# Kernel optimization log

Measured on AMD Instinct MI355X. Metric: run time of the kernel, lower is better.

Reference implementation:

```python
import jax, jax.numpy as jnp
import numpy as np

BATCH, T, N = 64, 512, 1024

def setup_inputs() -> dict:
    key = jax.random.key(0)
    k1, k2, k3 = jax.random.split(key, 3)
    input_sequence = jax.random.normal(k1, (BATCH, T, N), dtype=jnp.float32)
    W_self_lower = jax.random.normal(k2, (N, N), dtype=jnp.float32) * 0.1
    W_input = jax.random.normal(k3, (N, N), dtype=jnp.float32) * 0.1
    return {"input_sequence": input_sequence, "W_self_lower": W_self_lower, "W_input": W_input}

def reference(input_sequence, W_self_lower, W_input):
    # W_self symmetric: (W + W.T)/2; note W_self.T == W_self
    W_self = (W_self_lower + W_self_lower.T) * 0.5
    batch = input_sequence.shape[0]
    n = W_self.shape[0]
    # Precompute input projection for all timesteps: (B, T, N) @ (N, N)^T
    x_proj = jnp.einsum('btn,mn->btm', input_sequence, W_input)
    h0 = jnp.zeros((batch, n), dtype=input_sequence.dtype)

    def step(h, xp_t):
        h_new = jnp.tanh(h @ W_self.T + xp_t)
        return h_new, h_new

    # scan over time axis: move T to leading axis
    _, states = jax.lax.scan(step, h0, jnp.swapaxes(x_proj, 0, 1))
    return jnp.swapaxes(states, 0, 1)  # (B, T, N)
```

## Files before the change

kernel.cpp:

```cpp
#include <hip/hip_runtime.h>
#include <cstdint>
#include <cmath>

constexpr int BATCH = 64;
constexpr int T     = 512;
constexpr int N     = 1024;
constexpr int NWG   = 256;
constexpr int NG    = 32;
constexpr int GM    = 16;

typedef float f4 __attribute__((ext_vector_type(4)));
typedef float f2 __attribute__((ext_vector_type(2)));

struct alignas(128) PadInt { int v; int pad[31]; };
__device__ PadInt g_cnt[NG];
__device__ PadInt g_flag[NG];

__device__ __forceinline__ f4 ld_sys_x4(const float* p) {
  f4 v;
  asm volatile("global_load_dwordx4 %0, %1, off sc0 sc1" : "=v"(v) : "v"(p));
  return v;
}
__device__ __forceinline__ int ld_sys_i32(const int* p) {
  int v;
  asm volatile("global_load_dword %0, %1, off sc0 sc1\n\ts_waitcnt vmcnt(0)"
               : "=v"(v) : "v"(p) : "memory");
  return v;
}
__device__ __forceinline__ void st_sys_x2(float* p, f2 v) {
  asm volatile("global_store_dwordx2 %0, %1, off sc0 sc1 nt" ::"v"(p), "v"(v)
               : "memory");
}
__device__ __forceinline__ void wait_vm0(void) {
  asm volatile("s_waitcnt vmcnt(0)" ::: "memory");
  __builtin_amdgcn_sched_barrier(0);
}

__device__ __forceinline__ void arrive_cnt(int g, int t) {
  int old = __hip_atomic_fetch_add(&g_cnt[g].v, 1, __ATOMIC_RELAXED,
                                   __HIP_MEMORY_SCOPE_AGENT);
  if (old == t * GM + (GM - 1))
    __hip_atomic_store(&g_flag[g].v, t + 1, __ATOMIC_RELAXED,
                       __HIP_MEMORY_SCOPE_AGENT);
}
__device__ __forceinline__ void pollf(int g, int e) {
  while (ld_sys_i32(&g_flag[g].v) < e) __builtin_amdgcn_s_sleep(1);
}

__global__ __launch_bounds__(256) void symm_k(const float* __restrict__ W,
                                              float* __restrict__ Ws) {
  if (blockIdx.x == 0 && blockIdx.y == 0 && threadIdx.x < NG) {
    __hip_atomic_store(&g_cnt[threadIdx.x].v, 0, __ATOMIC_RELAXED,
                       __HIP_MEMORY_SCOPE_AGENT);
    __hip_atomic_store(&g_flag[threadIdx.x].v, 0, __ATOMIC_RELAXED,
                       __HIP_MEMORY_SCOPE_AGENT);
  }
  int j = blockIdx.x * 16 + (threadIdx.x & 15);
  int i = blockIdx.y * 16 + (threadIdx.x >> 4);
  Ws[(size_t)i * N + j] = 0.5f * (W[(size_t)i * N + j] + W[(size_t)j * N + i]);
}

__global__ __launch_bounds__(256) void xproj_gemm(const float* __restrict__ A,
                                                  const float* __restrict__ B,
                                                  float* __restrict__ C,
                                                  int M) {
  constexpr int BM = 128, BN = 128, BK = 16;
  __shared__ float As[BK][BM + 4];
  __shared__ float Bs[BK][BN + 4];

  const int tid = threadIdx.x;
  const int lin = blockIdx.x + gridDim.x * blockIdx.y;
  const int sw  = ((lin & 7) << 8) + (lin >> 3);
  const int bm  = sw >> 3;
  const int bn  = sw & 7;
  const int tx = tid & 15, ty = tid >> 4;
  const int K = N;

  float acc[8][8];
#pragma unroll
  for (int i = 0; i < 8; ++i)
#pragma unroll
    for (int j = 0; j < 8; ++j) acc[i][j] = 0.f;

  for (int kt = 0; kt < K; kt += BK) {
#pragma unroll
    for (int s = 0; s < 2; ++s) {
      int f = tid + s * 256;
      int row = f >> 2, kq = f & 3;
      float4 a = *reinterpret_cast<const float4*>(
          &A[(size_t)(bm * BM + row) * K + kt + kq * 4]);
      As[kq * 4 + 0][row] = a.x;
      As[kq * 4 + 1][row] = a.y;
      As[kq * 4 + 2][row] = a.z;
      As[kq * 4 + 3][row] = a.w;
      float4 b = *reinterpret_cast<const float4*>(
          &B[(size_t)(bn * BN + row) * K + kt + kq * 4]);
      Bs[kq * 4 + 0][row] = b.x;
      Bs[kq * 4 + 1][row] = b.y;
      Bs[kq * 4 + 2][row] = b.z;
      Bs[kq * 4 + 3][row] = b.w;
    }
    __syncthreads();

#pragma unroll
    for (int k = 0; k < BK; ++k) {
      float a[8], b[8];
      *reinterpret_cast<float4*>(&a[0]) =
          *reinterpret_cast<const float4*>(&As[k][ty * 8]);
      *reinterpret_cast<float4*>(&a[4]) =
          *reinterpret_cast<const float4*>(&As[k][ty * 8 + 4]);
      *reinterpret_cast<float4*>(&b[0]) =
          *reinterpret_cast<const float4*>(&Bs[k][tx * 8]);
      *reinterpret_cast<float4*>(&b[4]) =
          *reinterpret_cast<const float4*>(&Bs[k][tx * 8 + 4]);
#pragma unroll
      for (int i = 0; i < 8; ++i)
#pragma unroll
        for (int j = 0; j < 8; ++j) acc[i][j] = fmaf(a[i], b[j], acc[i][j]);
    }
    __syncthreads();
  }

#pragma unroll
  for (int i = 0; i < 8; ++i) {
    size_t row = (size_t)bm * BM + ty * 8 + i;
#pragma unroll
    for (int j = 0; j < 8; j += 4) {
      *reinterpret_cast<float4*>(&C[row * N + bn * BN + tx * 8 + j]) =
          *reinterpret_cast<const float4*>(&acc[i][j]);
    }
  }
}

__global__ __launch_bounds__(640, 1) void rnn_persist(
    float* __restrict__ out, const float* __restrict__ Ws) {
  const int tid = threadIdx.x;
  const int wg  = blockIdx.x;
  const int p   = wg & 15;
  const int cg  = wg >> 4;
  const int m0  = cg * 64;
  const int gA  = 2 * p, gB = 2 * p + 1;
  const int b0A = gA * 2, b0B = gB * 2;
  const size_t TN = (size_t)T * N;

  __shared__ __align__(16) char lds_raw[84992];
  __shared__ int lflags[64];
  float (*hA)[1028] = reinterpret_cast<float(*)[1028]>(lds_raw);
  float (*hB)[1028] = reinterpret_cast<float(*)[1028]>(lds_raw + 8224);
  float* xplA = reinterpret_cast<float*>(lds_raw + 16448);
  float* xplB = reinterpret_cast<float*>(lds_raw + 17024);
  float (*Wq)[1028] = reinterpret_cast<float(*)[1028]>(lds_raw);

  if (tid == 0) {
    lflags[0] = -1; lflags[16] = -1; lflags[32] = 0; lflags[48] = 0;
  }
  __syncthreads();

  const int l  = tid & 63;
  const int v  = tid >> 6;
  const int c2 = l & 3;
  const int kp = l >> 2;
  const int clocal = v * 8 + c2 * 2;

  f4 wreg[2][16];
  for (int quarter = 0; quarter < 8; ++quarter) {
    if (tid < 256) {
#pragma unroll
      for (int q = 0; q < 8; ++q)
        *reinterpret_cast<float4*>(&Wq[q][tid * 4]) =
            *reinterpret_cast<const float4*>(
                &Ws[(size_t)(m0 + quarter * 8 + q) * N + tid * 4]);
    }
    __syncthreads();
    if (v == quarter) {
#pragma unroll
      for (int ci = 0; ci < 2; ++ci)
#pragma unroll
        for (int j = 0; j < 16; ++j)
          wreg[ci][j] =
              *reinterpret_cast<const f4*>(&Wq[c2 * 2 + ci][kp * 4 + 64 * j]);
    }
    __syncthreads();
  }

  if (v < 8) {
    float* obA[2];
    float* obB[2];
#pragma unroll
    for (int bi = 0; bi < 2; ++bi) {
      obA[bi] = out + (size_t)(b0A + bi) * TN + m0 + clocal;
      obB[bi] = out + (size_t)(b0B + bi) * TN + m0 + clocal;
    }

    auto do_chain = [&](float (*hX)[1028], float* xplX, float* const* obX,
                        int rdyIdx, int cntIdx, int t) {
      while (*(volatile int*)&lflags[rdyIdx] < t) __builtin_amdgcn_s_sleep(1);
      __builtin_amdgcn_fence(__ATOMIC_ACQUIRE, "workgroup");
      float acc[4];
#pragma unroll
      for (int i = 0; i < 4; ++i) acc[i] = 0.f;
      if (t > 0) {
#pragma unroll
        for (int j = 0; j < 16; ++j) {
          const int kb = kp * 4 + 64 * j;
          f4 hv[2];
#pragma unroll
          for (int bi = 0; bi < 2; ++bi)
            hv[bi] = *reinterpret_cast<const f4*>(&hX[bi][kb]);
#pragma unroll
          for (int bi = 0; bi < 2; ++bi)
#pragma unroll
            for (int ci = 0; ci < 2; ++ci) {
              float a = acc[bi * 2 + ci];
              a = fmaf(hv[bi].x, wreg[ci][j].x, a);
              a = fmaf(hv[bi].y, wreg[ci][j].y, a);
              a = fmaf(hv[bi].z, wreg[ci][j].z, a);
              a = fmaf(hv[bi].w, wreg[ci][j].w, a);
              acc[bi * 2 + ci] = a;
            }
        }
#pragma unroll
        for (int o = 4; o < 64; o <<= 1)
#pragma unroll
          for (int i = 0; i < 4; ++i) acc[i] += __shfl_xor(acc[i], o, 64);
      }
      if (kp == 0) {
#pragma unroll
        for (int bi = 0; bi < 2; ++bi) {
          float x0 = xplX[bi * 64 + clocal];
          float x1 = xplX[bi * 64 + clocal + 1];
          f2 r;
          r.x = tanhf((t > 0 ? acc[bi * 2 + 0] : 0.f) + x0);
          r.y = tanhf((t > 0 ? acc[bi * 2 + 1] : 0.f) + x1);
          st_sys_x2(obX[bi] + (size_t)t * N, r);
        }
      }
      wait_vm0();
      if (l == 0) atomicAdd(&lflags[cntIdx], 1);
    };

    for (int t = 0; t < T; ++t) {
      do_chain(hA, xplA, obA, 0, 32, t);
      do_chain(hB, xplB, obB, 16, 48, t);
    }
  } else {
    const bool isB = (v == 9);
    const int lane = l;
    const int g    = isB ? gB : gA;
    const int b0   = isB ? b0B : b0A;
    float (*hb)[1028] = isB ? hB : hA;
    float* xpl = isB ? xplB : xplA;
    volatile int* ready = isB ? (volatile int*)&lflags[16]
                              : (volatile int*)&lflags[0];
    volatile int* cnt = isB ? (volatile int*)&lflags[48]
                            : (volatile int*)&lflags[32];

    const int r = lane >> 5;
    const int c = lane & 31;
    const float* hrow = out + (size_t)(b0 + r) * TN;
    const int xr = lane >> 4, xc = (lane & 15) * 4;
    const float* xsrc = out + (size_t)(b0 + xr) * TN + m0 + xc;

    f4 xnext;
    {
      f4 xv;
      if (lane < 32) xv = ld_sys_x4(xsrc);
      wait_vm0();
      if (lane < 32) *reinterpret_cast<f4*>(&xpl[xr * 64 + xc]) = xv;
      __builtin_amdgcn_fence(__ATOMIC_RELEASE, "workgroup");
      if (lane == 0) *ready = 0;
      if (lane < 32) xnext = ld_sys_x4(xsrc + (size_t)N);
    }

    for (int t = 1; t < T; ++t) {
      if (lane == 0) {
        while (*cnt < 8 * t) __builtin_amdgcn_s_sleep(1);
        arrive_cnt(g, t - 1);
        pollf(g, t);
      }
      const float* hs = hrow + (size_t)(t - 1) * N;
      f4 tmp[8];
#pragma unroll
      for (int q = 0; q < 8; ++q) tmp[q] = ld_sys_x4(hs + 4 * (c + 32 * q));
      wait_vm0();
#pragma unroll
      for (int q = 0; q < 8; ++q)
        *reinterpret_cast<f4*>(&hb[r][4 * (c + 32 * q)]) = tmp[q];
      if (lane < 32) *reinterpret_cast<f4*>(&xpl[xr * 64 + xc]) = xnext;
      __builtin_amdgcn_fence(__ATOMIC_RELEASE, "workgroup");
      if (lane == 0) *ready = t;
      if (t + 1 < T && lane < 32)
        xnext = ld_sys_x4(xsrc + (size_t)(t + 1) * N);
    }
  }
}

extern "C" void kernel_launch(void* const* d_in, const int* in_sizes, int n_in,
                              void* d_out, int out_size, void* d_ws,
                              size_t ws_size, hipStream_t stream) {
  const float* in_seq  = (const float*)d_in[0];
  const float* W_lower = (const float*)d_in[1];
  const float* W_input = (const float*)d_in[2];
  float* out = (float*)d_out;
  float* Ws  = (float*)d_ws;

  symm_k<<<dim3(N / 16, N / 16), 256, 0, stream>>>(W_lower, Ws);
  xproj_gemm<<<dim3(N / 128, (BATCH * T) / 128), 256, 0, stream>>>(
      in_seq, W_input, out, BATCH * T);
  rnn_persist<<<NWG, 640, 0, stream>>>(out, Ws);
}
```

Measured before the change: 2.949 ms.

## Use split-bf16 MFMA for recurrent matvec with cross-wave LDS reduction

Replaces the per-lane fp32 FMA dot products with bf16 MFMA 16x16x32 instructions. Weights and hidden state are each split into hi/lo bf16 parts, and four MFMAs per tile approximate fp32 accuracy. Each wave now covers a K-slice across all 64 output columns, so partial sums are reduced through LDS by wave 0, which applies tanh, stores the output and acks the loader. This puts more work on the matrix cores but adds an intra-workgroup LDS sync and a serial reduce/tanh/store step on one wave per timestep, on the critical latency path.

New measurement: 3.045 ms. +3.2%, slower.

```diff
diff --git a/kernel.cpp b/kernel.cpp
--- a/kernel.cpp
+++ b/kernel.cpp
@@ -1,4 +1,5 @@
 #include <hip/hip_runtime.h>
+#include <hip/hip_bf16.h>
 #include <cstdint>
 #include <cmath>
 
@@ -10,7 +11,7 @@
 constexpr int GM    = 16;
 
 typedef float f4 __attribute__((ext_vector_type(4)));
-typedef float f2 __attribute__((ext_vector_type(2)));
+typedef short bs8 __attribute__((ext_vector_type(8)));
 
 struct alignas(128) PadInt { int v; int pad[31]; };
 __device__ PadInt g_cnt[NG];
@@ -27,8 +28,8 @@
                : "=v"(v) : "v"(p) : "memory");
   return v;
 }
-__device__ __forceinline__ void st_sys_x2(float* p, f2 v) {
-  asm volatile("global_store_dwordx2 %0, %1, off sc0 sc1 nt" ::"v"(p), "v"(v)
+__device__ __forceinline__ void st_sys_f32(float* p, float v) {
+  asm volatile("global_store_dword %0, %1, off sc0 sc1 nt" ::"v"(p), "v"(v)
                : "memory");
 }
 __device__ __forceinline__ void wait_vm0(void) {
@@ -45,6 +46,33 @@
 }
 __device__ __forceinline__ void pollf(int g, int e) {
   while (ld_sys_i32(&g_flag[g].v) < e) __builtin_amdgcn_s_sleep(1);
+}
+
+__device__ __forceinline__ unsigned short f2bf(float f) {
+  unsigned u = __builtin_bit_cast(unsigned, f);
+  u = u + 0x7FFFu + ((u >> 16) & 1u);
+  return (unsigned short)(u >> 16);
+}
+__device__ __forceinline__ float bf2f(unsigned short b) {
+  unsigned u = ((unsigned)b) << 16;
+  return __builtin_bit_cast(float, u);
+}
+__device__ __forceinline__ bs8 mk8hi(const float* p) {
+  bs8 r;
+#pragma unroll
+  for (int j = 0; j < 8; ++j) r[j] = (short)f2bf(p[j]);
+  return r;
+}
+__device__ __forceinline__ void mk8hilo(const float* p, bs8& hi, bs8& lo) {
+  f4 a = *reinterpret_cast<const f4*>(p);
+  f4 b = *reinterpret_cast<const f4*>(p + 4);
+  float v[8] = {a[0], a[1], a[2], a[3], b[0], b[1], b[2], b[3]};
+#pragma unroll
+  for (int j = 0; j < 8; ++j) {
+    unsigned short h = f2bf(v[j]);
+    hi[j] = (short)h;
+    lo[j] = (short)f2bf(v[j] - bf2f(h));
+  }
 }
 
 __global__ __launch_bounds__(256) void symm_k(const float* __restrict__ W,
@@ -143,105 +171,114 @@
   const int b0A = gA * 2, b0B = gB * 2;
   const size_t TN = (size_t)T * N;
 
-  __shared__ __align__(16) char lds_raw[84992];
+  __shared__ __align__(16) short wloL[64][1032];
+  __shared__ __align__(16) float hA[2][1028];
+  __shared__ __align__(16) float hB[2][1028];
+  __shared__ float xplA[128], xplB[128];
+  __shared__ float redA[8 * 128], redB[8 * 128];
   __shared__ int lflags[64];
-  float (*hA)[1028] = reinterpret_cast<float(*)[1028]>(lds_raw);
-  float (*hB)[1028] = reinterpret_cast<float(*)[1028]>(lds_raw + 8224);
-  float* xplA = reinterpret_cast<float*>(lds_raw + 16448);
-  float* xplB = reinterpret_cast<float*>(lds_raw + 17024);
-  float (*Wq)[1028] = reinterpret_cast<float(*)[1028]>(lds_raw);
 
   if (tid == 0) {
-    lflags[0] = -1; lflags[16] = -1; lflags[32] = 0; lflags[48] = 0;
+    lflags[0] = -1; lflags[16] = -1;
+    lflags[8] = 0;  lflags[24] = 0;
+    lflags[32] = 0; lflags[48] = 0;
+  }
+
+  const int l = tid & 63;
+  const int v = tid >> 6;
+
+  for (int e = tid; e < 64 * 1024; e += 640) {
+    int row = e >> 10, k = e & 1023;
+    float x = Ws[(size_t)(m0 + row) * N + k];
+    unsigned short hi = f2bf(x);
+    wloL[row][k] = (short)f2bf(x - bf2f(hi));
+  }
+  bs8 whi[4][4];
+  if (v < 8) {
+#pragma unroll
+    for (int mt = 0; mt < 4; ++mt)
+#pragma unroll
+      for (int kt = 0; kt < 4; ++kt)
+        whi[mt][kt] = mk8hi(
+            &Ws[(size_t)(m0 + 16 * mt + (l & 15)) * N + 128 * v + 32 * kt +
+                8 * (l >> 4)]);
   }
   __syncthreads();
 
-  const int l  = tid & 63;
-  const int v  = tid >> 6;
-  const int c2 = l & 3;
-  const int kp = l >> 2;
-  const int clocal = v * 8 + c2 * 2;
-
-  f4 wreg[2][16];
-  for (int quarter = 0; quarter < 8; ++quarter) {
-    if (tid < 256) {
-#pragma unroll
-      for (int q = 0; q < 8; ++q)
-        *reinterpret_cast<float4*>(&Wq[q][tid * 4]) =
-            *reinterpret_cast<const float4*>(
-                &Ws[(size_t)(m0 + quarter * 8 + q) * N + tid * 4]);
-    }
-    __syncthreads();
-    if (v == quarter) {
-#pragma unroll
-      for (int ci = 0; ci < 2; ++ci)
-#pragma unroll
-        for (int j = 0; j < 16; ++j)
-          wreg[ci][j] =
-              *reinterpret_cast<const f4*>(&Wq[c2 * 2 + ci][kp * 4 + 64 * j]);
-    }
-    __syncthreads();
-  }
-
   if (v < 8) {
-    float* obA[2];
-    float* obB[2];
-#pragma unroll
-    for (int bi = 0; bi < 2; ++bi) {
-      obA[bi] = out + (size_t)(b0A + bi) * TN + m0 + clocal;
-      obB[bi] = out + (size_t)(b0B + bi) * TN + m0 + clocal;
-    }
-
-    auto do_chain = [&](float (*hX)[1028], float* xplX, float* const* obX,
-                        int rdyIdx, int cntIdx, int t) {
+    const int n = l & 15;
+    const int koff = 128 * v + 8 * (l >> 4);
+
+    auto do_chain = [&](float (*hX)[1028], float* xplX, float* redX,
+                        int rdyIdx, int wsIdx, int ackIdx, int b0, int t) {
       while (*(volatile int*)&lflags[rdyIdx] < t) __builtin_amdgcn_s_sleep(1);
       __builtin_amdgcn_fence(__ATOMIC_ACQUIRE, "workgroup");
-      float acc[4];
-#pragma unroll
-      for (int i = 0; i < 4; ++i) acc[i] = 0.f;
       if (t > 0) {
-#pragma unroll
-        for (int j = 0; j < 16; ++j) {
-          const int kb = kp * 4 + 64 * j;
-          f4 hv[2];
-#pragma unroll
-          for (int bi = 0; bi < 2; ++bi)
-            hv[bi] = *reinterpret_cast<const f4*>(&hX[bi][kb]);
-#pragma unroll
-          for (int bi = 0; bi < 2; ++bi)
-#pragma unroll
-            for (int ci = 0; ci < 2; ++ci) {
-              float a = acc[bi * 2 + ci];
-              a = fmaf(hv[bi].x, wreg[ci][j].x, a);
-              a = fmaf(hv[bi].y, wreg[ci][j].y, a);
-              a = fmaf(hv[bi].z, wreg[ci][j].z, a);
-              a = fmaf(hv[bi].w, wreg[ci][j].w, a);
-              acc[bi * 2 + ci] = a;
-            }
+        const float* hrow_ = &hX[n & 1][0];
+        f4 acc0 = {0.f, 0.f, 0.f, 0.f}, acc1 = {0.f, 0.f, 0.f, 0.f};
+        f4 acc2 = {0.f, 0.f, 0.f, 0.f}, acc3 = {0.f, 0.f, 0.f, 0.f};
+#pragma unroll
+        for (int kt = 0; kt < 4; ++kt) {
+          bs8 bhi, blo;
+          mk8hilo(hrow_ + koff + 32 * kt, bhi, blo);
+          bs8 wl0 = *reinterpret_cast<const bs8*>(&wloL[n][koff + 32 * kt]);
+          bs8 wl1 = *reinterpret_cast<const bs8*>(&wloL[16 + n][koff + 32 * kt]);
+          bs8 wl2 = *reinterpret_cast<const bs8*>(&wloL[32 + n][koff + 32 * kt]);
+          bs8 wl3 = *reinterpret_cast<const bs8*>(&wloL[48 + n][koff + 32 * kt]);
+          acc0 = __builtin_amdgcn_mfma_f32_16x16x32_bf16(whi[0][kt], bhi, acc0, 0, 0, 0);
+          acc0 = __builtin_amdgcn_mfma_f32_16x16x32_bf16(whi[0][kt], blo, acc0, 0, 0, 0);
+          acc0 = __builtin_amdgcn_mfma_f32_16x16x32_bf16(wl0, bhi, acc0, 0, 0, 0);
+          acc0 = __builtin_amdgcn_mfma_f32_16x16x32_bf16(wl0, blo, acc0, 0, 0, 0);
+          acc1 = __builtin_amdgcn_mfma_f32_16x16x32_bf16(whi[1][kt], bhi, acc1, 0, 0, 0);
+          acc1 = __builtin_amdgcn_mfma_f32_16x16x32_bf16(whi[1][kt], blo, acc1, 0, 0, 0);
+          acc1 = __builtin_amdgcn_mfma_f32_16x16x32_bf16(wl1, bhi, acc1, 0, 0, 0);
+          acc1 = __builtin_amdgcn_mfma_f32_16x16x32_bf16(wl1, blo, acc1, 0, 0, 0);
+          acc2 = __builtin_amdgcn_mfma_f32_16x16x32_bf16(whi[2][kt], bhi, acc2, 0, 0, 0);
+          acc2 = __builtin_amdgcn_mfma_f32_16x16x32_bf16(whi[2][kt], blo, acc2, 0, 0, 0);
+          acc2 = __builtin_amdgcn_mfma_f32_16x16x32_bf16(wl2, bhi, acc2, 0, 0, 0);
+          acc2 = __builtin_amdgcn_mfma_f32_16x16x32_bf16(wl2, blo, acc2, 0, 0, 0);
+          acc3 = __builtin_amdgcn_mfma_f32_16x16x32_bf16(whi[3][kt], bhi, acc3, 0, 0, 0);
+          acc3 = __builtin_amdgcn_mfma_f32_16x16x32_bf16(whi[3][kt], blo, acc3, 0, 0, 0);
+          acc3 = __builtin_amdgcn_mfma_f32_16x16x32_bf16(wl3, bhi, acc3, 0, 0, 0);
+          acc3 = __builtin_amdgcn_mfma_f32_16x16x32_bf16(wl3, blo, acc3, 0, 0, 0);
         }
-#pragma unroll
-        for (int o = 4; o < 64; o <<= 1)
-#pragma unroll
-          for (int i = 0; i < 4; ++i) acc[i] += __shfl_xor(acc[i], o, 64);
-      }
-      if (kp == 0) {
-#pragma unroll
-        for (int bi = 0; bi < 2; ++bi) {
-          float x0 = xplX[bi * 64 + clocal];
-          float x1 = xplX[bi * 64 + clocal + 1];
-          f2 r;
-          r.x = tanhf((t > 0 ? acc[bi * 2 + 0] : 0.f) + x0);
-          r.y = tanhf((t > 0 ? acc[bi * 2 + 1] : 0.f) + x1);
-          st_sys_x2(obX[bi] + (size_t)t * N, r);
+        if (n < 2) {
+          const int rb = 4 * (l >> 4);
+#pragma unroll
+          for (int r = 0; r < 4; ++r) {
+            redX[v * 128 + (0  + rb + r) * 2 + n] = acc0[r];
+            redX[v * 128 + (16 + rb + r) * 2 + n] = acc1[r];
+            redX[v * 128 + (32 + rb + r) * 2 + n] = acc2[r];
+            redX[v * 128 + (48 + rb + r) * 2 + n] = acc3[r];
+          }
         }
       }
-      wait_vm0();
-      if (l == 0) atomicAdd(&lflags[cntIdx], 1);
+      __builtin_amdgcn_fence(__ATOMIC_RELEASE, "workgroup");
+      if (l == 0) atomicAdd(&lflags[wsIdx], 1);
+      if (v == 0) {
+        while (*(volatile int*)&lflags[wsIdx] < 8 * (t + 1))
+          __builtin_amdgcn_s_sleep(1);
+        __builtin_amdgcn_fence(__ATOMIC_ACQUIRE, "workgroup");
+        float pre0 = 0.f, pre1 = 0.f;
+        if (t > 0) {
+#pragma unroll
+          for (int w = 0; w < 8; ++w) {
+            pre0 += redX[w * 128 + l * 2 + 0];
+            pre1 += redX[w * 128 + l * 2 + 1];
+          }
+        }
+        float h0 = tanhf(pre0 + xplX[l]);
+        float h1 = tanhf(pre1 + xplX[64 + l]);
+        st_sys_f32(out + (size_t)(b0 + 0) * TN + (size_t)t * N + m0 + l, h0);
+        st_sys_f32(out + (size_t)(b0 + 1) * TN + (size_t)t * N + m0 + l, h1);
+        wait_vm0();
+        if (l == 0) atomicAdd(&lflags[ackIdx], 1);
+      }
     };
 
     for (int t = 0; t < T; ++t) {
-      do_chain(hA, xplA, obA, 0, 32, t);
-      do_chain(hB, xplB, obB, 16, 48, t);
+      do_chain(hA, xplA, redA, 0, 8, 32, b0A, t);
+      do_chain(hB, xplB, redB, 16, 24, 48, b0B, t);
     }
   } else {
     const bool isB = (v == 9);
@@ -274,7 +311,7 @@
 
     for (int t = 1; t < T; ++t) {
       if (lane == 0) {
-        while (*cnt < 8 * t) __builtin_amdgcn_s_sleep(1);
+        while (*cnt < t) __builtin_amdgcn_s_sleep(1);
         arrive_cnt(g, t - 1);
         pollf(g, t);
       }
```
